# Optimization experiments

Hardware: AMD Instinct MI355X
Metric: run time of the kernel (lower is better)

## Reference

```python
import jax, jax.numpy as jnp
import numpy as np

# ---- PUMA functional-model constants (module globals / resolved defaults) ----
XBAR_ROW, XBAR_COL = 128, 128
BIT_SLICE, BIT_STREAM = 2, 1
WEIGHT_BITS, W_FRAC = 16, 12          # weight_bit_frac = weight_bits//4*3
INPUT_BITS, I_FRAC = 16, 12           # input_bit_frac  = input_bits//4*3
ACM_BITS, ACM_FRAC = 16, 12
ADC_BIT = int(np.log2(XBAR_ROW)) + BIT_SLICE   # 7 + 2 = 9 (bit_stream==1 branch)
N_SLICE = WEIGHT_BITS // BIT_SLICE             # 8 weight slices, MSB first in columns
N_STREAM = INPUT_BITS // BIT_STREAM            # 16 input bit-streams, LSB first

B, IN_F, OUT_F = 64, 1024, 1024


def setup_inputs() -> dict:
    key = jax.random.key(0)
    k1, k2, k3 = jax.random.split(key, 3)
    x = jax.random.normal(k1, (B, IN_F), dtype=jnp.float32)
    weight = jax.random.normal(k2, (OUT_F, IN_F), dtype=jnp.float32) * 0.05
    bias = jax.random.uniform(k3, (OUT_F,), dtype=jnp.float32, minval=-0.1, maxval=0.1)
    return {"x": x, "weight": weight, "bias": bias}


def _bit_slice_weight(w):
    # w: [O, I] non-negative magnitudes. Fixed-point (W_FRAC frac bits), then split
    # into N_SLICE slices of BIT_SLICE bits, MSB first. Returns [I, O*N_SLICE]:
    # each output column occupies N_SLICE contiguous crossbar columns.
    wint = jnp.clip(jnp.round(w * (2.0 ** W_FRAC)), 0.0, 2.0 ** WEIGHT_BITS - 1.0)
    shifts = 2.0 ** (BIT_SLICE * jnp.arange(N_SLICE - 1, -1, -1, dtype=jnp.float32))
    sl = jnp.floor(wint[:, :, None] / shifts) % (2.0 ** BIT_SLICE)   # [O, I, N_SLICE]
    return sl.transpose(1, 0, 2).reshape(w.shape[1], w.shape[0] * N_SLICE)


def _to_xbars(sliced):
    # Zero-pad to the 128x128 crossbar grid and tile: -> [xr, xc, R, C]
    rows, cols = sliced.shape
    xr, xc = -(-rows // XBAR_ROW), -(-cols // XBAR_COL)
    padded = jnp.zeros((xr * XBAR_ROW, xc * XBAR_COL), sliced.dtype).at[:rows, :cols].set(sliced)
    return padded.reshape(xr, XBAR_ROW, xc, XBAR_COL).transpose(0, 2, 1, 3)


def _binarize_input(x, xr):
    # Two's-complement fixed point, bits LSB-first along last dim (stream i = bit i;
    # the final MSB stream carries weight -2^(INPUT_BITS-1)). -> [B, xr, R, N_STREAM]
    xi = jnp.clip(jnp.round(x * 2.0 ** I_FRAC),
                  -2.0 ** (INPUT_BITS - 1), 2.0 ** (INPUT_BITS - 1) - 1)
    xi = jnp.where(xi < 0, xi + 2.0 ** INPUT_BITS, xi)
    shifts = 2.0 ** jnp.arange(INPUT_BITS, dtype=jnp.float32)
    bits = jnp.floor(xi[:, :, None] / shifts) % 2.0                  # [B, I, N_STREAM]
    full = jnp.zeros((x.shape[0], xr * XBAR_ROW, N_STREAM), x.dtype).at[:, :x.shape[1]].set(bits)
    return full.reshape(x.shape[0], xr, XBAR_ROW, N_STREAM)


def _mvm_polarity(bits, xbars):
    # bits: [B, xr, R, S] binary input streams; xbars: [xr, xc, R, C] weight slices.
    # Analog crossbar MAC per stream, ADC clamp, slice shift-add, stream shift-add.
    analog = jnp.einsum('brns,rcnm->brcsm', bits, xbars)             # [B,xr,xc,S,C]
    analog = jnp.clip(jnp.round(analog), 0.0, 2.0 ** ADC_BIT - 1.0)  # ADC quantization
    Bn, xr, xc, S, C = analog.shape
    analog = analog.reshape(Bn, xr, xc, S, C // N_SLICE, N_SLICE)
    slice_w = 2.0 ** (BIT_SLICE * jnp.arange(N_SLICE - 1, -1, -1, dtype=jnp.float32))
    reg = jnp.einsum('brcsok,k->brcso', analog, slice_w)             # shift-add slices
    stream_w = (2.0 ** jnp.arange(N_STREAM, dtype=jnp.float32)).at[-1].multiply(-1.0)
    out = jnp.einsum('brcso,s->brco', reg, stream_w).sum(1)          # + sum row tiles
    out = out.reshape(Bn, -1) * 2.0 ** (-(W_FRAC + I_FRAC))
    # accumulator fixed-point quantization
    out = jnp.clip(jnp.round(out * 2.0 ** ACM_FRAC),
                   -2.0 ** (ACM_BITS - 1), 2.0 ** (ACM_BITS - 1) - 1) * 2.0 ** (-ACM_FRAC)
    return out


def reference(x, weight, bias):
    pos = _to_xbars(_bit_slice_weight(jnp.clip(weight, 0.0, None)))
    neg = _to_xbars(_bit_slice_weight(jnp.abs(jnp.clip(weight, None, 0.0))))
    bits = _binarize_input(x, pos.shape[0])
    out = _mvm_polarity(bits, pos) - _mvm_polarity(bits, neg)
    return out[:, :OUT_F] + bias[None, :]
```

## Files before the change

### kernel.cpp

```cpp
#include <hip/hip_runtime.h>
#include <hip/hip_bf16.h>
#include <stdint.h>


#define WS_XQ_OFF (4u * 1024u * 1024u)

typedef short short2v __attribute__((ext_vector_type(2)));

__device__ __forceinline__ uint32_t packw(float w) {
    float p = __builtin_rintf(fmaxf(w, 0.0f) * 4096.0f);
    float n = __builtin_rintf(fmaxf(-w, 0.0f) * 4096.0f);
    p = fminf(p, 65535.0f);
    n = fminf(n, 65535.0f);
    return (uint32_t)p | ((uint32_t)n << 16);
}

__device__ __forceinline__ int qx(float v) {
    float q = __builtin_rintf(v * 4096.0f);
    return (int)fminf(fmaxf(q, -32768.0f), 32767.0f);
}

__global__ __launch_bounds__(256) void quant_kernel(
        const float* __restrict__ w, const float* __restrict__ x,
        uint32_t* __restrict__ packedW, uint32_t* __restrict__ xq) {
    const int bid = blockIdx.x;
    const int tid = threadIdx.x;
    if (bid < 256) {
        __shared__ uint32_t lds[64][69];
        const int to = (bid >> 4) * 64;
        const int ti = (bid & 15) * 64;
        const int r = tid >> 4;
        const int c = (tid & 15) * 4;
        #pragma unroll
        for (int it = 0; it < 4; ++it) {
            const int ol = r + it * 16;
            const float4 wv = *(const float4*)(w + (size_t)(to + ol) * 1024 + ti + c);
            lds[ol][c + 0] = packw(wv.x);
            lds[ol][c + 1] = packw(wv.y);
            lds[ol][c + 2] = packw(wv.z);
            lds[ol][c + 3] = packw(wv.w);
        }
        __syncthreads();
        const int ol = tid & 63;
        const int wq = tid >> 6;
        #pragma unroll
        for (int it = 0; it < 16; ++it) {
            const int il = wq + it * 4;
            packedW[(size_t)(ti + il) * 1024 + to + ol] = lds[ol][il];
        }
    } else {
        const int xb = bid - 256;
        uint32_t* __restrict__ dst = xq + xb * 2048;
        #pragma unroll
        for (int pp = 0; pp < 2; ++pp) {
            const int p = pp * 256 + tid;
            uint32_t v0, v1, v2, v3;
            {
                const float2 a = *(const float2*)(x + (size_t)(xb * 4 + 0) * 1024 + p * 2);
                v0 = ((uint32_t)qx(a.x) & 0xFFFFu) | ((uint32_t)qx(a.y) << 16);
            }
            {
                const float2 a = *(const float2*)(x + (size_t)(xb * 4 + 1) * 1024 + p * 2);
                v1 = ((uint32_t)qx(a.x) & 0xFFFFu) | ((uint32_t)qx(a.y) << 16);
            }
            {
                const float2 a = *(const float2*)(x + (size_t)(xb * 4 + 2) * 1024 + p * 2);
                v2 = ((uint32_t)qx(a.x) & 0xFFFFu) | ((uint32_t)qx(a.y) << 16);
            }
            {
                const float2 a = *(const float2*)(x + (size_t)(xb * 4 + 3) * 1024 + p * 2);
                v3 = ((uint32_t)qx(a.x) & 0xFFFFu) | ((uint32_t)qx(a.y) << 16);
            }
            *(uint4*)(dst + p * 4) = make_uint4(v0, v1, v2, v3);
        }
    }
}

__global__ __launch_bounds__(1024) void mvm_kernel(
        const uint32_t* __restrict__ packedW, const uint32_t* __restrict__ xq,
        const float* __restrict__ bias, float* __restrict__ out) {
    __shared__ int xs[2048];
    __shared__ long long red[8][8][64];

    const int tid = threadIdx.x;
    const int bid = blockIdx.x;
    const int o_t = bid & 15;
    const int b_t = bid >> 4;
    const int o_l = tid & 63;
    const int c = tid >> 6;
    const int o = o_t * 64 + o_l;

    if (tid < 512)
        *(int4*)(xs + tid * 4) = *(const int4*)(xq + (size_t)b_t * 2048 + tid * 4);
    __syncthreads();

    const uint32_t* __restrict__ wp = packedW + (size_t)(c * 64) * 1024 + o;
    const int* __restrict__ xp = xs + c * 128;

    int apl[4] = {0, 0, 0, 0}, aph[4] = {0, 0, 0, 0};
    int anl[4] = {0, 0, 0, 0}, anh[4] = {0, 0, 0, 0};

    #pragma unroll 4
    for (int p = 0; p < 32; ++p) {
        const uint32_t wv0 = wp[(p * 2 + 0) * 1024];
        const uint32_t wv1 = wp[(p * 2 + 1) * 1024];
        const uint32_t wPL = (wv0 & 0xFFu)          | ((wv1 & 0xFFu) << 16);
        const uint32_t wPH = ((wv0 >> 8) & 0xFFu)   | (((wv1 >> 8) & 0xFFu) << 16);
        const uint32_t wNL = ((wv0 >> 16) & 0xFFu)  | (((wv1 >> 16) & 0xFFu) << 16);
        const uint32_t wNH = (wv0 >> 24)            | ((wv1 >> 24) << 16);
        const int4 xv = *(const int4*)(xp + p * 4);
#if __has_builtin(__builtin_amdgcn_sdot2)
        const short2v sPL = __builtin_bit_cast(short2v, wPL);
        const short2v sPH = __builtin_bit_cast(short2v, wPH);
        const short2v sNL = __builtin_bit_cast(short2v, wNL);
        const short2v sNH = __builtin_bit_cast(short2v, wNH);
        {
            const short2v xa = __builtin_bit_cast(short2v, xv.x);
            apl[0] = __builtin_amdgcn_sdot2(xa, sPL, apl[0], false);
            aph[0] = __builtin_amdgcn_sdot2(xa, sPH, aph[0], false);
            anl[0] = __builtin_amdgcn_sdot2(xa, sNL, anl[0], false);
            anh[0] = __builtin_amdgcn_sdot2(xa, sNH, anh[0], false);
        }
        {
            const short2v xa = __builtin_bit_cast(short2v, xv.y);
            apl[1] = __builtin_amdgcn_sdot2(xa, sPL, apl[1], false);
            aph[1] = __builtin_amdgcn_sdot2(xa, sPH, aph[1], false);
            anl[1] = __builtin_amdgcn_sdot2(xa, sNL, anl[1], false);
            anh[1] = __builtin_amdgcn_sdot2(xa, sNH, anh[1], false);
        }
        {
            const short2v xa = __builtin_bit_cast(short2v, xv.z);
            apl[2] = __builtin_amdgcn_sdot2(xa, sPL, apl[2], false);
            aph[2] = __builtin_amdgcn_sdot2(xa, sPH, aph[2], false);
            anl[2] = __builtin_amdgcn_sdot2(xa, sNL, anl[2], false);
            anh[2] = __builtin_amdgcn_sdot2(xa, sNH, anh[2], false);
        }
        {
            const short2v xa = __builtin_bit_cast(short2v, xv.w);
            apl[3] = __builtin_amdgcn_sdot2(xa, sPL, apl[3], false);
            aph[3] = __builtin_amdgcn_sdot2(xa, sPH, aph[3], false);
            anl[3] = __builtin_amdgcn_sdot2(xa, sNL, anl[3], false);
            anh[3] = __builtin_amdgcn_sdot2(xa, sNH, anh[3], false);
        }
#else
        const int pl0 = (int)(wv0 & 255u), pl1 = (int)(wv1 & 255u);
        const int ph0 = (int)((wv0 >> 8) & 255u), ph1 = (int)((wv1 >> 8) & 255u);
        const int nl0 = (int)((wv0 >> 16) & 255u), nl1 = (int)((wv1 >> 16) & 255u);
        const int nh0 = (int)(wv0 >> 24), nh1 = (int)(wv1 >> 24);
        {
            const int xe = (int)(short)(xv.x & 0xFFFF), xo = xv.x >> 16;
            apl[0] += __mul24(xe, pl0) + __mul24(xo, pl1);
            aph[0] += __mul24(xe, ph0) + __mul24(xo, ph1);
            anl[0] += __mul24(xe, nl0) + __mul24(xo, nl1);
            anh[0] += __mul24(xe, nh0) + __mul24(xo, nh1);
        }
        {
            const int xe = (int)(short)(xv.y & 0xFFFF), xo = xv.y >> 16;
            apl[1] += __mul24(xe, pl0) + __mul24(xo, pl1);
            aph[1] += __mul24(xe, ph0) + __mul24(xo, ph1);
            anl[1] += __mul24(xe, nl0) + __mul24(xo, nl1);
            anh[1] += __mul24(xe, nh0) + __mul24(xo, nh1);
        }
        {
            const int xe = (int)(short)(xv.z & 0xFFFF), xo = xv.z >> 16;
            apl[2] += __mul24(xe, pl0) + __mul24(xo, pl1);
            aph[2] += __mul24(xe, ph0) + __mul24(xo, ph1);
            anl[2] += __mul24(xe, nl0) + __mul24(xo, nl1);
            anh[2] += __mul24(xe, nh0) + __mul24(xo, nh1);
        }
        {
            const int xe = (int)(short)(xv.w & 0xFFFF), xo = xv.w >> 16;
            apl[3] += __mul24(xe, pl0) + __mul24(xo, pl1);
            aph[3] += __mul24(xe, ph0) + __mul24(xo, ph1);
            anl[3] += __mul24(xe, nl0) + __mul24(xo, nl1);
            anh[3] += __mul24(xe, nh0) + __mul24(xo, nh1);
        }
#endif
    }

    long long pp[4], pn[4];
    #pragma unroll
    for (int b = 0; b < 4; ++b) {
        pp[b] = (long long)apl[b] + ((long long)aph[b] << 8);
        pn[b] = (long long)anl[b] + ((long long)anh[b] << 8);
    }

    if (c >= 8) {
        #pragma unroll
        for (int b = 0; b < 4; ++b) {
            red[b * 2 + 0][c - 8][o_l] = pp[b];
            red[b * 2 + 1][c - 8][o_l] = pn[b];
        }
    }
    __syncthreads();
    if (c < 8) {
        #pragma unroll
        for (int b = 0; b < 4; ++b) {
            red[b * 2 + 0][c][o_l] += pp[b];
            red[b * 2 + 1][c][o_l] += pn[b];
        }
    }
    __syncthreads();

    if (tid < 256) {
        const int ro = tid & 63;
        const int rb = tid >> 6;
        long long ap = 0, an = 0;
        #pragma unroll
        for (int cc = 0; cc < 8; ++cc) {
            ap += red[rb * 2 + 0][cc][ro];
            an += red[rb * 2 + 1][cc][ro];
        }
        double qp = rint((double)ap * (1.0 / 4096.0));
        qp = fmin(fmax(qp, -32768.0), 32767.0);
        double qn = rint((double)an * (1.0 / 4096.0));
        qn = fmin(fmax(qn, -32768.0), 32767.0);
        const int oo = o_t * 64 + ro;
        out[(size_t)(b_t * 4 + rb) * 1024 + oo] =
            (float)((qp - qn) * (1.0 / 4096.0)) + bias[oo];
    }
}

extern "C" void kernel_launch(void* const* d_in, const int* in_sizes, int n_in,
                              void* d_out, int out_size, void* d_ws, size_t ws_size,
                              hipStream_t stream) {
    const float* x    = (const float*)d_in[0];
    const float* w    = (const float*)d_in[1];
    const float* bias = (const float*)d_in[2];
    float* out = (float*)d_out;

    uint32_t* packedW = (uint32_t*)d_ws;
    uint32_t* xq = (uint32_t*)((char*)d_ws + WS_XQ_OFF);

    quant_kernel<<<272, 256, 0, stream>>>(w, x, packedW, xq);
    mvm_kernel<<<256, 1024, 0, stream>>>(packedW, xq, bias, out);
}
```

Baseline: 71.70 us.

## Halve batch rows per MVM block and double block count

The MVM kernel now handles 2 batch rows per block instead of 4, using 512 threads with 8 input chunks of 128 rows each, and launches 512 blocks instead of 256. The quantized-x layout is rearranged into pairs of batch rows to match. The goal is more blocks across the CUs and lower per-thread register pressure, for better occupancy. The cost is that each weight load is reused for only 2 batch rows, which doubles total weight traffic from L2.

```diff
diff --git a/kernel.cpp b/kernel.cpp
--- a/kernel.cpp
+++ b/kernel.cpp
@@ -50,7 +50,8 @@
         }
     } else {
         const int xb = bid - 256;
-        uint32_t* __restrict__ dst = xq + xb * 2048;
+        uint32_t* __restrict__ dst0 = xq + (size_t)(xb * 2 + 0) * 1024;
+        uint32_t* __restrict__ dst1 = xq + (size_t)(xb * 2 + 1) * 1024;
         #pragma unroll
         for (int pp = 0; pp < 2; ++pp) {
             const int p = pp * 256 + tid;
@@ -71,16 +72,17 @@
                 const float2 a = *(const float2*)(x + (size_t)(xb * 4 + 3) * 1024 + p * 2);
                 v3 = ((uint32_t)qx(a.x) & 0xFFFFu) | ((uint32_t)qx(a.y) << 16);
             }
-            *(uint4*)(dst + p * 4) = make_uint4(v0, v1, v2, v3);
-        }
-    }
-}
-
-__global__ __launch_bounds__(1024) void mvm_kernel(
+            *(uint2*)(dst0 + p * 2) = make_uint2(v0, v1);
+            *(uint2*)(dst1 + p * 2) = make_uint2(v2, v3);
+        }
+    }
+}
+
+__global__ __launch_bounds__(512, 4) void mvm_kernel(
         const uint32_t* __restrict__ packedW, const uint32_t* __restrict__ xq,
         const float* __restrict__ bias, float* __restrict__ out) {
-    __shared__ int xs[2048];
-    __shared__ long long red[8][8][64];
+    __shared__ int xs[1024];
+    __shared__ long long red[4][4][64];
 
     const int tid = threadIdx.x;
     const int bid = blockIdx.x;
@@ -90,25 +92,25 @@
     const int c = tid >> 6;
     const int o = o_t * 64 + o_l;
 
-    if (tid < 512)
-        *(int4*)(xs + tid * 4) = *(const int4*)(xq + (size_t)b_t * 2048 + tid * 4);
+    if (tid < 256)
+        *(int4*)(xs + tid * 4) = *(const int4*)((const int*)xq + (size_t)b_t * 1024 + tid * 4);
     __syncthreads();
 
-    const uint32_t* __restrict__ wp = packedW + (size_t)(c * 64) * 1024 + o;
+    const uint32_t* __restrict__ wp = packedW + (size_t)(c * 128) * 1024 + o;
     const int* __restrict__ xp = xs + c * 128;
 
-    int apl[4] = {0, 0, 0, 0}, aph[4] = {0, 0, 0, 0};
-    int anl[4] = {0, 0, 0, 0}, anh[4] = {0, 0, 0, 0};
+    int apl[2] = {0, 0}, aph[2] = {0, 0};
+    int anl[2] = {0, 0}, anh[2] = {0, 0};
 
     #pragma unroll 4
-    for (int p = 0; p < 32; ++p) {
-        const uint32_t wv0 = wp[(p * 2 + 0) * 1024];
-        const uint32_t wv1 = wp[(p * 2 + 1) * 1024];
+    for (int j = 0; j < 64; ++j) {
+        const uint32_t wv0 = wp[(size_t)(j * 2 + 0) * 1024];
+        const uint32_t wv1 = wp[(size_t)(j * 2 + 1) * 1024];
         const uint32_t wPL = (wv0 & 0xFFu)          | ((wv1 & 0xFFu) << 16);
         const uint32_t wPH = ((wv0 >> 8) & 0xFFu)   | (((wv1 >> 8) & 0xFFu) << 16);
         const uint32_t wNL = ((wv0 >> 16) & 0xFFu)  | (((wv1 >> 16) & 0xFFu) << 16);
         const uint32_t wNH = (wv0 >> 24)            | ((wv1 >> 24) << 16);
-        const int4 xv = *(const int4*)(xp + p * 4);
+        const int2 xv = *(const int2*)(xp + j * 2);
 #if __has_builtin(__builtin_amdgcn_sdot2)
         const short2v sPL = __builtin_bit_cast(short2v, wPL);
         const short2v sPH = __builtin_bit_cast(short2v, wPH);
@@ -128,20 +130,6 @@
             anl[1] = __builtin_amdgcn_sdot2(xa, sNL, anl[1], false);
             anh[1] = __builtin_amdgcn_sdot2(xa, sNH, anh[1], false);
         }
-        {
-            const short2v xa = __builtin_bit_cast(short2v, xv.z);
-            apl[2] = __builtin_amdgcn_sdot2(xa, sPL, apl[2], false);
-            aph[2] = __builtin_amdgcn_sdot2(xa, sPH, aph[2], false);
-            anl[2] = __builtin_amdgcn_sdot2(xa, sNL, anl[2], false);
-            anh[2] = __builtin_amdgcn_sdot2(xa, sNH, anh[2], false);
-        }
-        {
-            const short2v xa = __builtin_bit_cast(short2v, xv.w);
-            apl[3] = __builtin_amdgcn_sdot2(xa, sPL, apl[3], false);
-            aph[3] = __builtin_amdgcn_sdot2(xa, sPH, aph[3], false);
-            anl[3] = __builtin_amdgcn_sdot2(xa, sNL, anl[3], false);
-            anh[3] = __builtin_amdgcn_sdot2(xa, sNH, anh[3], false);
-        }
 #else
         const int pl0 = (int)(wv0 & 255u), pl1 = (int)(wv1 & 255u);
         const int ph0 = (int)((wv0 >> 8) & 255u), ph1 = (int)((wv1 >> 8) & 255u);
@@ -161,53 +149,39 @@
             anl[1] += __mul24(xe, nl0) + __mul24(xo, nl1);
             anh[1] += __mul24(xe, nh0) + __mul24(xo, nh1);
         }
-        {
-            const int xe = (int)(short)(xv.z & 0xFFFF), xo = xv.z >> 16;
-            apl[2] += __mul24(xe, pl0) + __mul24(xo, pl1);
-            aph[2] += __mul24(xe, ph0) + __mul24(xo, ph1);
-            anl[2] += __mul24(xe, nl0) + __mul24(xo, nl1);
-            anh[2] += __mul24(xe, nh0) + __mul24(xo, nh1);
-        }
-        {
-            const int xe = (int)(short)(xv.w & 0xFFFF), xo = xv.w >> 16;
-            apl[3] += __mul24(xe, pl0) + __mul24(xo, pl1);
-            aph[3] += __mul24(xe, ph0) + __mul24(xo, ph1);
-            anl[3] += __mul24(xe, nl0) + __mul24(xo, nl1);
-            anh[3] += __mul24(xe, nh0) + __mul24(xo, nh1);
-        }
 #endif
     }
 
-    long long pp[4], pn[4];
+    long long pp[2], pn[2];
     #pragma unroll
-    for (int b = 0; b < 4; ++b) {
+    for (int b = 0; b < 2; ++b) {
         pp[b] = (long long)apl[b] + ((long long)aph[b] << 8);
         pn[b] = (long long)anl[b] + ((long long)anh[b] << 8);
     }
 
-    if (c >= 8) {
-        #pragma unroll
-        for (int b = 0; b < 4; ++b) {
-            red[b * 2 + 0][c - 8][o_l] = pp[b];
-            red[b * 2 + 1][c - 8][o_l] = pn[b];
+    if (c >= 4) {
+        #pragma unroll
+        for (int b = 0; b < 2; ++b) {
+            red[b * 2 + 0][c - 4][o_l] = pp[b];
+            red[b * 2 + 1][c - 4][o_l] = pn[b];
         }
     }
     __syncthreads();
-    if (c < 8) {
-        #pragma unroll
-        for (int b = 0; b < 4; ++b) {
+    if (c < 4) {
+        #pragma unroll
+        for (int b = 0; b < 2; ++b) {
             red[b * 2 + 0][c][o_l] += pp[b];
             red[b * 2 + 1][c][o_l] += pn[b];
         }
     }
     __syncthreads();
 
-    if (tid < 256) {
+    if (tid < 128) {
         const int ro = tid & 63;
         const int rb = tid >> 6;
         long long ap = 0, an = 0;
         #pragma unroll
-        for (int cc = 0; cc < 8; ++cc) {
+        for (int cc = 0; cc < 4; ++cc) {
             ap += red[rb * 2 + 0][cc][ro];
             an += red[rb * 2 + 1][cc][ro];
         }
@@ -216,7 +190,7 @@
         double qn = rint((double)an * (1.0 / 4096.0));
         qn = fmin(fmax(qn, -32768.0), 32767.0);
         const int oo = o_t * 64 + ro;
-        out[(size_t)(b_t * 4 + rb) * 1024 + oo] =
+        out[(size_t)(b_t * 2 + rb) * 1024 + oo] =
             (float)((qp - qn) * (1.0 / 4096.0)) + bias[oo];
     }
 }
@@ -233,5 +207,5 @@
     uint32_t* xq = (uint32_t*)((char*)d_ws + WS_XQ_OFF);
 
     quant_kernel<<<272, 256, 0, stream>>>(w, x, packedW, xq);
-    mvm_kernel<<<256, 1024, 0, stream>>>(packedW, xq, bias, out);
-}
+    mvm_kernel<<<512, 512, 0, stream>>>(packedW, xq, bias, out);
+}
```

After: 73.74 us. +2.8%, slower.
